# Kernel tuning notes

Hardware: AMD Instinct MI355X
Metric: run time of the kernel (lower is better)

## Reference

```python
import jax, jax.numpy as jnp
import numpy as np

B, S, D, V = 2, 2048, 1024, 32000
EPSILON = 5.0


def setup_inputs() -> dict:
    key = jax.random.key(0)
    k1, k2, k3, k4 = jax.random.split(key, 4)
    inputs_embeds = jax.random.normal(k1, (B, S, D), dtype=jnp.float32)
    table = jax.random.normal(k2, (V, D), dtype=jnp.float32)
    # dx-privacy noise: unit-norm Gaussian direction * Gamma(alpha=D, rate=eps*D) scalar sample
    noise_v = jax.random.normal(k3, (B, S, D), dtype=jnp.float32)
    norm = jnp.linalg.norm(noise_v, axis=-1, keepdims=True)
    norm = jnp.where(norm > 0, norm, jnp.ones_like(norm))
    gamma_scale = jax.random.gamma(k4, jnp.float32(D)) / jnp.float32(EPSILON * D)
    noise = gamma_scale * (noise_v / norm)
    return {"inputs_embeds": inputs_embeds, "table": table, "noise": noise}


def reference(inputs_embeds, table, noise):
    # perturb embeddings with precomputed dx-privacy noise (no_grad in original)
    perturbed = inputs_embeds + noise                      # [B,S,D]
    # full similarity matrix vs vocabulary, then nearest-embedding snap
    sims = jnp.einsum('bsd,vd->bsv', perturbed, table)     # [B,S,V]
    max_token = jnp.argmax(sims, axis=-1)                  # [B,S] int
    res = jnp.take(table, max_token, axis=0)               # [B,S,D]
    return res
```

## Files before the change

kernel.cpp:

```cpp
#include <hip/hip_runtime.h>
#include <stdint.h>

#define ROWS 4096
#define DIM 1024
#define VOCAB 32000
#define BM 128
#define BN 128
#define NTILES (VOCAB / BN)
#define NCHUNKS 24
#define SCALE 2048.0f

typedef float floatx4 __attribute__((ext_vector_type(4)));
typedef _Float16 f16x8 __attribute__((ext_vector_type(8)));
typedef _Float16 f16x4 __attribute__((ext_vector_type(4)));

__device__ __forceinline__ void load_lds16(const _Float16* g, _Float16* l) {
    __builtin_amdgcn_global_load_lds(
        (const __attribute__((address_space(1))) uint32_t*)g,
        (__attribute__((address_space(3))) uint32_t*)l, 16, 0, 0);
}

__global__ void init_keys(unsigned long long* __restrict__ keys) {
    int i = blockIdx.x * 256 + threadIdx.x;
    if (i < ROWS) keys[i] = 0ull;
}

__global__ void split_sum(const float* __restrict__ x, const float* __restrict__ y,
                          _Float16* __restrict__ hi, _Float16* __restrict__ lo) {
    size_t i = ((size_t)blockIdx.x * 256 + threadIdx.x) * 8;
    floatx4 a = *(const floatx4*)(x + i);
    floatx4 b = *(const floatx4*)(x + i + 4);
    floatx4 c = *(const floatx4*)(y + i);
    floatx4 d = *(const floatx4*)(y + i + 4);
    f16x8 h, l;
#pragma unroll
    for (int j = 0; j < 4; j++) {
        float p = (a[j] + c[j]) * SCALE;
        _Float16 hh = (_Float16)p;
        h[j] = hh; l[j] = (_Float16)(p - (float)hh);
        float q = (b[j] + d[j]) * SCALE;
        _Float16 hq = (_Float16)q;
        h[4 + j] = hq; l[4 + j] = (_Float16)(q - (float)hq);
    }
    *(f16x8*)(hi + i) = h;
    *(f16x8*)(lo + i) = l;
}

__global__ void split_one(const float* __restrict__ x,
                          _Float16* __restrict__ hi, _Float16* __restrict__ lo) {
    size_t i = ((size_t)blockIdx.x * 256 + threadIdx.x) * 8;
    floatx4 a = *(const floatx4*)(x + i);
    floatx4 b = *(const floatx4*)(x + i + 4);
    f16x8 h, l;
#pragma unroll
    for (int j = 0; j < 4; j++) {
        float p = a[j] * SCALE;
        _Float16 hh = (_Float16)p;
        h[j] = hh; l[j] = (_Float16)(p - (float)hh);
        float q = b[j] * SCALE;
        _Float16 hq = (_Float16)q;
        h[4 + j] = hq; l[4 + j] = (_Float16)(q - (float)hq);
    }
    *(f16x8*)(hi + i) = h;
    *(f16x8*)(lo + i) = l;
}

__global__ __launch_bounds__(256, 3) void gemm_argmax_pre(
    const _Float16* __restrict__ Ah, const _Float16* __restrict__ Al,
    const _Float16* __restrict__ Bh, const _Float16* __restrict__ Bl,
    unsigned long long* __restrict__ keys) {
    __shared__ __align__(16) _Float16 sAh[BM * 32];
    __shared__ __align__(16) _Float16 sAl[BM * 32];
    __shared__ __align__(16) _Float16 sBh[BN * 32];
    __shared__ __align__(16) _Float16 sBl[BN * 32];
    __shared__ unsigned long long redk[BM];

    const int tid = threadIdx.x;
    const int w = tid >> 6, lane = tid & 63;
    const int quad = lane >> 4, lq = lane & 15;
    const int rb = blockIdx.x / NCHUNKS, chunk = blockIdx.x % NCHUNKS;
    const int row0 = rb * BM;
    const int wm = (w & 1) * 64, wn = (w >> 1) * 64;
    const int tstart = chunk * NTILES / NCHUNKS;
    const int tend = (chunk + 1) * NTILES / NCHUNKS;

    if (tid < BM) redk[tid] = 0ull;

    union PF { f16x8 v; _Float16 s[8]; } fidx, fone;
#pragma unroll
    for (int j = 0; j < 8; j++) { fidx.s[j] = (_Float16)0.0f; fone.s[j] = (_Float16)0.0f; }
    if (quad == 0) { fidx.s[0] = (_Float16)(float)lq; fone.s[0] = (_Float16)1.0f; }
    floatx4 c1 = {0.f, 0.f, 0.f, 0.f}, c2 = {0.f, 0.f, 0.f, 0.f};
    c1 = __builtin_amdgcn_mfma_f32_16x16x32_f16(fidx.v, fone.v, c1, 0, 0, 0);
    c2 = __builtin_amdgcn_mfma_f32_16x16x32_f16(fone.v, fidx.v, c2, 0, 0, 0);
    int m_of[4], n_of[4];
#pragma unroll
    for (int r = 0; r < 4; r++) {
        m_of[r] = (int)(c1[r] + 0.5f);
        n_of[r] = (int)(c2[r] + 0.5f);
    }

    const _Float16* gsrcA = (w == 0) ? (Ah + (size_t)row0 * DIM)
                        : (w == 1) ? (Al + (size_t)row0 * DIM)
                        : (w == 2) ? Bh : Bl;
    _Float16* ldst = (w == 0) ? sAh : (w == 1) ? sAl : (w == 2) ? sBh : sBl;

    float rmax[16];
    int ridx[16];
#pragma unroll
    for (int i = 0; i < 16; i++) { rmax[i] = -3.4e38f; ridx[i] = 0; }

    for (int t = tstart; t < tend; ++t) {
        const int n0 = t * BN;
        const _Float16* gsrc = (w < 2) ? gsrcA : (gsrcA + (size_t)n0 * DIM);
        floatx4 acc[4][4];
#pragma unroll
        for (int mi = 0; mi < 4; mi++)
#pragma unroll
            for (int ni = 0; ni < 4; ni++)
#pragma unroll
                for (int r = 0; r < 4; r++) acc[mi][ni][r] = 0.0f;

        for (int kt = 0; kt < DIM / 32; ++kt) {
            const int k0 = kt * 32;
            __syncthreads();
#pragma unroll
            for (int c = 0; c < 8; c++) {
                const _Float16* g =
                    gsrc + (size_t)(c * 16 + (lane >> 2)) * DIM + k0 + (lane & 3) * 8;
                load_lds16(g, ldst + c * 512);
            }
            __syncthreads();

            f16x8 ahf[4], alf[4];
#pragma unroll
            for (int i = 0; i < 4; i++) {
                int r = wm + i * 16 + lq;
                ahf[i] = *(const f16x8*)(sAh + r * 32 + quad * 8);
                alf[i] = *(const f16x8*)(sAl + r * 32 + quad * 8);
            }
#pragma unroll
            for (int ni = 0; ni < 4; ni++) {
                int r = wn + ni * 16 + lq;
                f16x8 bh = *(const f16x8*)(sBh + r * 32 + quad * 8);
                f16x8 bl = *(const f16x8*)(sBl + r * 32 + quad * 8);
#pragma unroll
                for (int mi = 0; mi < 4; mi++) {
                    acc[mi][ni] = __builtin_amdgcn_mfma_f32_16x16x32_f16(
                        ahf[mi], bh, acc[mi][ni], 0, 0, 0);
                    acc[mi][ni] = __builtin_amdgcn_mfma_f32_16x16x32_f16(
                        ahf[mi], bl, acc[mi][ni], 0, 0, 0);
                    acc[mi][ni] = __builtin_amdgcn_mfma_f32_16x16x32_f16(
                        alf[mi], bh, acc[mi][ni], 0, 0, 0);
                }
            }
        }
#pragma unroll
        for (int mi = 0; mi < 4; mi++)
#pragma unroll
            for (int ni = 0; ni < 4; ni++)
#pragma unroll
                for (int r = 0; r < 4; r++) {
                    float v = acc[mi][ni][r];
                    int col = n0 + wn + ni * 16 + n_of[r];
                    int s = mi * 4 + r;
                    if (v > rmax[s] || (v == rmax[s] && col < ridx[s])) {
                        rmax[s] = v;
                        ridx[s] = col;
                    }
                }
    }

#pragma unroll
    for (int s = 0; s < 16; ++s) {
        int mi = s >> 2, r = s & 3;
        int rowl = wm + mi * 16 + m_of[r];
        union { float f; uint32_t i; } u;
        u.f = rmax[s];
        uint32_t ord = (u.i & 0x80000000u) ? ~u.i : (u.i | 0x80000000u);
        unsigned long long key =
            ((unsigned long long)ord << 32) | (uint32_t)(~(uint32_t)ridx[s]);
        atomicMax(&redk[rowl], key);
    }
    __syncthreads();
    if (tid < BM) atomicMax(&keys[row0 + tid], redk[tid]);
}

#define BKF 64
#define LDKF 72
#define TILES_PER_WGF 10
#define NCHUNKSF 25

__global__ __launch_bounds__(256, 2) void gemm_argmax_fused(
    const float* __restrict__ emb, const float* __restrict__ noi,
    const float* __restrict__ table, unsigned long long* __restrict__ keys) {
    __shared__ __align__(16) _Float16 Ah[BM * LDKF];
    __shared__ __align__(16) _Float16 Al[BM * LDKF];
    __shared__ __align__(16) _Float16 Bh[BN * LDKF];
    __shared__ __align__(16) _Float16 Bl[BN * LDKF];
    __shared__ unsigned long long redk[BM];

    const int tid = threadIdx.x;
    const int wave = tid >> 6, lane = tid & 63;
    const int quad = lane >> 4, lq = lane & 15;
    const int rb = blockIdx.x / NCHUNKSF, chunk = blockIdx.x % NCHUNKSF;
    const int row0 = rb * BM;
    const int wm = (wave & 1) * 64, wn = (wave >> 1) * 64;

    if (tid < BM) redk[tid] = 0ull;

    union PF { f16x8 v; _Float16 s[8]; } fidx, fone;
#pragma unroll
    for (int j = 0; j < 8; j++) { fidx.s[j] = (_Float16)0.0f; fone.s[j] = (_Float16)0.0f; }
    if (quad == 0) { fidx.s[0] = (_Float16)(float)lq; fone.s[0] = (_Float16)1.0f; }
    floatx4 c1 = {0.f, 0.f, 0.f, 0.f}, c2 = {0.f, 0.f, 0.f, 0.f};
    c1 = __builtin_amdgcn_mfma_f32_16x16x32_f16(fidx.v, fone.v, c1, 0, 0, 0);
    c2 = __builtin_amdgcn_mfma_f32_16x16x32_f16(fone.v, fidx.v, c2, 0, 0, 0);
    int m_of[4], n_of[4];
#pragma unroll
    for (int r = 0; r < 4; r++) {
        m_of[r] = (int)(c1[r] + 0.5f);
        n_of[r] = (int)(c2[r] + 0.5f);
    }

    float rmax[16];
    int ridx[16];
#pragma unroll
    for (int i = 0; i < 16; i++) { rmax[i] = -3.4e38f; ridx[i] = 0; }

    for (int t = 0; t < TILES_PER_WGF; ++t) {
        const int n0 = (chunk * TILES_PER_WGF + t) * BN;
        floatx4 acc[4][4];
#pragma unroll
        for (int mi = 0; mi < 4; mi++)
#pragma unroll
            for (int ni = 0; ni < 4; ni++)
#pragma unroll
                for (int r = 0; r < 4; r++) acc[mi][ni][r] = 0.0f;

        for (int kt = 0; kt < DIM / BKF; ++kt) {
            const int k0 = kt * BKF;
            __syncthreads();
#pragma unroll
            for (int i = 0; i < 8; i++) {
                int c = i * 256 + tid;
                int r = c >> 4, q = c & 15;
                floatx4 e = *(const floatx4*)(emb + (size_t)(row0 + r) * DIM + k0 + q * 4);
                floatx4 n = *(const floatx4*)(noi + (size_t)(row0 + r) * DIM + k0 + q * 4);
                floatx4 b = *(const floatx4*)(table + (size_t)(n0 + r) * DIM + k0 + q * 4);
                f16x4 ah, al, bh, bl;
#pragma unroll
                for (int j = 0; j < 4; j++) {
                    float pa = (e[j] + n[j]) * SCALE;
                    _Float16 h = (_Float16)pa;
                    ah[j] = h;
                    al[j] = (_Float16)(pa - (float)h);
                    float pb = b[j] * SCALE;
                    _Float16 hb = (_Float16)pb;
                    bh[j] = hb;
                    bl[j] = (_Float16)(pb - (float)hb);
                }
                *(f16x4*)(Ah + r * LDKF + q * 4) = ah;
                *(f16x4*)(Al + r * LDKF + q * 4) = al;
                *(f16x4*)(Bh + r * LDKF + q * 4) = bh;
                *(f16x4*)(Bl + r * LDKF + q * 4) = bl;
            }
            __syncthreads();
#pragma unroll
            for (int ks = 0; ks < BKF; ks += 32) {
                f16x8 bhf[4], blf[4], ahf[4], alf[4];
#pragma unroll
                for (int i = 0; i < 4; i++) {
                    bhf[i] = *(const f16x8*)(Bh + (wn + i * 16 + lq) * LDKF + ks + quad * 8);
                    blf[i] = *(const f16x8*)(Bl + (wn + i * 16 + lq) * LDKF + ks + quad * 8);
                    ahf[i] = *(const f16x8*)(Ah + (wm + i * 16 + lq) * LDKF + ks + quad * 8);
                    alf[i] = *(const f16x8*)(Al + (wm + i * 16 + lq) * LDKF + ks + quad * 8);
                }
#pragma unroll
                for (int mi = 0; mi < 4; mi++)
#pragma unroll
                    for (int ni = 0; ni < 4; ni++) {
                        acc[mi][ni] = __builtin_amdgcn_mfma_f32_16x16x32_f16(
                            ahf[mi], bhf[ni], acc[mi][ni], 0, 0, 0);
                        acc[mi][ni] = __builtin_amdgcn_mfma_f32_16x16x32_f16(
                            ahf[mi], blf[ni], acc[mi][ni], 0, 0, 0);
                        acc[mi][ni] = __builtin_amdgcn_mfma_f32_16x16x32_f16(
                            alf[mi], bhf[ni], acc[mi][ni], 0, 0, 0);
                    }
            }
        }
#pragma unroll
        for (int mi = 0; mi < 4; mi++)
#pragma unroll
            for (int ni = 0; ni < 4; ni++)
#pragma unroll
                for (int r = 0; r < 4; r++) {
                    float v = acc[mi][ni][r];
                    int col = n0 + wn + ni * 16 + n_of[r];
                    int s = mi * 4 + r;
                    if (v > rmax[s] || (v == rmax[s] && col < ridx[s])) {
                        rmax[s] = v;
                        ridx[s] = col;
                    }
                }
    }

#pragma unroll
    for (int s = 0; s < 16; ++s) {
        int mi = s >> 2, r = s & 3;
        int rowl = wm + mi * 16 + m_of[r];
        union { float f; uint32_t i; } u;
        u.f = rmax[s];
        uint32_t ord = (u.i & 0x80000000u) ? ~u.i : (u.i | 0x80000000u);
        unsigned long long key =
            ((unsigned long long)ord << 32) | (uint32_t)(~(uint32_t)ridx[s]);
        atomicMax(&redk[rowl], key);
    }
    __syncthreads();
    if (tid < BM) atomicMax(&keys[row0 + tid], redk[tid]);
}

__global__ void gather_kernel(const unsigned long long* __restrict__ keys,
                              const float* __restrict__ table,
                              float* __restrict__ out) {
    int row = blockIdx.x;
    unsigned long long key = keys[row];
    uint32_t ix = ~(uint32_t)(key & 0xFFFFFFFFull);
    const floatx4* src = (const floatx4*)(table + (size_t)ix * DIM);
    floatx4* dst = (floatx4*)(out + (size_t)row * DIM);
    dst[threadIdx.x] = src[threadIdx.x];
}

extern "C" void kernel_launch(void* const* d_in, const int* in_sizes, int n_in,
                              void* d_out, int out_size, void* d_ws, size_t ws_size,
                              hipStream_t stream) {
    (void)in_sizes; (void)n_in; (void)out_size;
    const float* emb = (const float*)d_in[0];
    const float* table = (const float*)d_in[1];
    const float* noi = (const float*)d_in[2];
    float* out = (float*)d_out;

    uint8_t* ws = (uint8_t*)d_ws;
    unsigned long long* keys = (unsigned long long*)ws;
    const size_t keysB = (size_t)ROWS * 8;
    const size_t aB = (size_t)ROWS * DIM * 2;
    const size_t bB = (size_t)VOCAB * DIM * 2;
    const size_t need = keysB + 2 * aB + 2 * bB;

    init_keys<<<ROWS / 256, 256, 0, stream>>>(keys);

    if (ws_size >= need) {
        _Float16* Ah = (_Float16*)(ws + keysB);
        _Float16* Al = (_Float16*)(ws + keysB + aB);
        _Float16* Bh = (_Float16*)(ws + keysB + 2 * aB);
        _Float16* Bl = (_Float16*)(ws + keysB + 2 * aB + bB);
        split_sum<<<ROWS * DIM / 8 / 256, 256, 0, stream>>>(emb, noi, Ah, Al);
        split_one<<<VOCAB * DIM / 8 / 256, 256, 0, stream>>>(table, Bh, Bl);
        gemm_argmax_pre<<<(ROWS / BM) * NCHUNKS, 256, 0, stream>>>(Ah, Al, Bh, Bl, keys);
    } else {
        gemm_argmax_fused<<<(ROWS / BM) * NCHUNKSF, 256, 0, stream>>>(emb, noi, table, keys);
    }
    gather_kernel<<<ROWS, 256, 0, stream>>>(keys, table, out);
}
```

Before: 1.016 ms.

## Swizzle LDS layout, merge split kernels, raise occupancy and chunk count

Applies an XOR swizzle to the global-to-LDS load addresses and the matching fragment reads, so the 16-byte LDS reads of the 32-wide rows spread across banks. The three preprocessing kernels (key init, split of activations, split of table) become one launch. Occupancy hint rises from 3 to 4 waves-groups per CU and the vocab split per row block goes from 24 to 32 chunks. Together these aim to cut LDS bank conflicts, launch overhead and tail imbalance, at the cost of register pressure under the tighter launch bound and more atomic merges.

```diff
diff --git a/kernel.cpp b/kernel.cpp
--- a/kernel.cpp
+++ b/kernel.cpp
@@ -7,7 +7,7 @@
 #define BM 128
 #define BN 128
 #define NTILES (VOCAB / BN)
-#define NCHUNKS 24
+#define NCHUNKS 32
 #define SCALE 2048.0f
 
 typedef float floatx4 __attribute__((ext_vector_type(4)));
@@ -20,52 +20,56 @@
         (__attribute__((address_space(3))) uint32_t*)l, 16, 0, 0);
 }
 
-__global__ void init_keys(unsigned long long* __restrict__ keys) {
-    int i = blockIdx.x * 256 + threadIdx.x;
-    if (i < ROWS) keys[i] = 0ull;
-}
-
-__global__ void split_sum(const float* __restrict__ x, const float* __restrict__ y,
-                          _Float16* __restrict__ hi, _Float16* __restrict__ lo) {
-    size_t i = ((size_t)blockIdx.x * 256 + threadIdx.x) * 8;
-    floatx4 a = *(const floatx4*)(x + i);
-    floatx4 b = *(const floatx4*)(x + i + 4);
-    floatx4 c = *(const floatx4*)(y + i);
-    floatx4 d = *(const floatx4*)(y + i + 4);
-    f16x8 h, l;
-#pragma unroll
-    for (int j = 0; j < 4; j++) {
-        float p = (a[j] + c[j]) * SCALE;
-        _Float16 hh = (_Float16)p;
-        h[j] = hh; l[j] = (_Float16)(p - (float)hh);
-        float q = (b[j] + d[j]) * SCALE;
-        _Float16 hq = (_Float16)q;
-        h[4 + j] = hq; l[4 + j] = (_Float16)(q - (float)hq);
-    }
-    *(f16x8*)(hi + i) = h;
-    *(f16x8*)(lo + i) = l;
-}
-
-__global__ void split_one(const float* __restrict__ x,
-                          _Float16* __restrict__ hi, _Float16* __restrict__ lo) {
-    size_t i = ((size_t)blockIdx.x * 256 + threadIdx.x) * 8;
-    floatx4 a = *(const floatx4*)(x + i);
-    floatx4 b = *(const floatx4*)(x + i + 4);
-    f16x8 h, l;
-#pragma unroll
-    for (int j = 0; j < 4; j++) {
-        float p = a[j] * SCALE;
-        _Float16 hh = (_Float16)p;
-        h[j] = hh; l[j] = (_Float16)(p - (float)hh);
-        float q = b[j] * SCALE;
-        _Float16 hq = (_Float16)q;
-        h[4 + j] = hq; l[4 + j] = (_Float16)(q - (float)hq);
-    }
-    *(f16x8*)(hi + i) = h;
-    *(f16x8*)(lo + i) = l;
-}
-
-__global__ __launch_bounds__(256, 3) void gemm_argmax_pre(
+__global__ void split_all(const float* __restrict__ emb, const float* __restrict__ noi,
+                          const float* __restrict__ table,
+                          _Float16* __restrict__ Ah, _Float16* __restrict__ Al,
+                          _Float16* __restrict__ Bh, _Float16* __restrict__ Bl,
+                          unsigned long long* __restrict__ keys) {
+    int b = blockIdx.x;
+    if (b < 16) {
+        keys[b * 256 + threadIdx.x] = 0ull;
+        return;
+    }
+    b -= 16;
+    if (b < 2048) {
+        size_t i = ((size_t)b * 256 + threadIdx.x) * 8;
+        floatx4 a = *(const floatx4*)(emb + i);
+        floatx4 bb = *(const floatx4*)(emb + i + 4);
+        floatx4 c = *(const floatx4*)(noi + i);
+        floatx4 d = *(const floatx4*)(noi + i + 4);
+        f16x8 h, l;
+#pragma unroll
+        for (int j = 0; j < 4; j++) {
+            float p = (a[j] + c[j]) * SCALE;
+            _Float16 hh = (_Float16)p;
+            h[j] = hh; l[j] = (_Float16)(p - (float)hh);
+            float q = (bb[j] + d[j]) * SCALE;
+            _Float16 hq = (_Float16)q;
+            h[4 + j] = hq; l[4 + j] = (_Float16)(q - (float)hq);
+        }
+        *(f16x8*)(Ah + i) = h;
+        *(f16x8*)(Al + i) = l;
+    } else {
+        b -= 2048;
+        size_t i = ((size_t)b * 256 + threadIdx.x) * 8;
+        floatx4 a = *(const floatx4*)(table + i);
+        floatx4 bb = *(const floatx4*)(table + i + 4);
+        f16x8 h, l;
+#pragma unroll
+        for (int j = 0; j < 4; j++) {
+            float p = a[j] * SCALE;
+            _Float16 hh = (_Float16)p;
+            h[j] = hh; l[j] = (_Float16)(p - (float)hh);
+            float q = bb[j] * SCALE;
+            _Float16 hq = (_Float16)q;
+            h[4 + j] = hq; l[4 + j] = (_Float16)(q - (float)hq);
+        }
+        *(f16x8*)(Bh + i) = h;
+        *(f16x8*)(Bl + i) = l;
+    }
+}
+
+__global__ __launch_bounds__(256, 4) void gemm_argmax_pre(
     const _Float16* __restrict__ Ah, const _Float16* __restrict__ Al,
     const _Float16* __restrict__ Bh, const _Float16* __restrict__ Bl,
     unsigned long long* __restrict__ keys) {
@@ -84,6 +88,10 @@
     const int tstart = chunk * NTILES / NCHUNKS;
     const int tend = (chunk + 1) * NTILES / NCHUNKS;
 
+    const int qsw = (lane & 3) ^ ((lane >> 2) & 3) ^ ((lane >> 4) & 3);
+    const int grow = lane >> 2;
+    const int psw = (quad ^ (lq & 3) ^ ((lq >> 2) & 3)) * 8;
+
     if (tid < BM) redk[tid] = 0ull;
 
     union PF { f16x8 v; _Float16 s[8]; } fidx, fone;
@@ -127,7 +135,7 @@
 #pragma unroll
             for (int c = 0; c < 8; c++) {
                 const _Float16* g =
-                    gsrc + (size_t)(c * 16 + (lane >> 2)) * DIM + k0 + (lane & 3) * 8;
+                    gsrc + (size_t)(c * 16 + grow) * DIM + k0 + qsw * 8;
                 load_lds16(g, ldst + c * 512);
             }
             __syncthreads();
@@ -136,14 +144,14 @@
 #pragma unroll
             for (int i = 0; i < 4; i++) {
                 int r = wm + i * 16 + lq;
-                ahf[i] = *(const f16x8*)(sAh + r * 32 + quad * 8);
-                alf[i] = *(const f16x8*)(sAl + r * 32 + quad * 8);
+                ahf[i] = *(const f16x8*)(sAh + r * 32 + psw);
+                alf[i] = *(const f16x8*)(sAl + r * 32 + psw);
             }
 #pragma unroll
             for (int ni = 0; ni < 4; ni++) {
                 int r = wn + ni * 16 + lq;
-                f16x8 bh = *(const f16x8*)(sBh + r * 32 + quad * 8);
-                f16x8 bl = *(const f16x8*)(sBl + r * 32 + quad * 8);
+                f16x8 bh = *(const f16x8*)(sBh + r * 32 + psw);
+                f16x8 bl = *(const f16x8*)(sBl + r * 32 + psw);
 #pragma unroll
                 for (int mi = 0; mi < 4; mi++) {
                     acc[mi][ni] = __builtin_amdgcn_mfma_f32_16x16x32_f16(
@@ -191,6 +199,11 @@
 #define TILES_PER_WGF 10
 #define NCHUNKSF 25
 
+__global__ void init_keys(unsigned long long* __restrict__ keys) {
+    int i = blockIdx.x * 256 + threadIdx.x;
+    if (i < ROWS) keys[i] = 0ull;
+}
+
 __global__ __launch_bounds__(256, 2) void gemm_argmax_fused(
     const float* __restrict__ emb, const float* __restrict__ noi,
     const float* __restrict__ table, unsigned long long* __restrict__ keys) {
@@ -347,17 +360,16 @@
     const size_t bB = (size_t)VOCAB * DIM * 2;
     const size_t need = keysB + 2 * aB + 2 * bB;
 
-    init_keys<<<ROWS / 256, 256, 0, stream>>>(keys);
-
     if (ws_size >= need) {
         _Float16* Ah = (_Float16*)(ws + keysB);
         _Float16* Al = (_Float16*)(ws + keysB + aB);
         _Float16* Bh = (_Float16*)(ws + keysB + 2 * aB);
         _Float16* Bl = (_Float16*)(ws + keysB + 2 * aB + bB);
-        split_sum<<<ROWS * DIM / 8 / 256, 256, 0, stream>>>(emb, noi, Ah, Al);
-        split_one<<<VOCAB * DIM / 8 / 256, 256, 0, stream>>>(table, Bh, Bl);
+        split_all<<<16 + 2048 + 16000, 256, 0, stream>>>(emb, noi, table,
+                                                         Ah, Al, Bh, Bl, keys);
         gemm_argmax_pre<<<(ROWS / BM) * NCHUNKS, 256, 0, stream>>>(Ah, Al, Bh, Bl, keys);
     } else {
+        init_keys<<<ROWS / 256, 256, 0, stream>>>(keys);
         gemm_argmax_fused<<<(ROWS / BM) * NCHUNKSF, 256, 0, stream>>>(emb, noi, table, keys);
     }
     gather_kernel<<<ROWS, 256, 0, stream>>>(keys, table, out);
```

Measured after the change: 1.111 ms. 1.09x slower.
